# Performance work log

Measured on AMD Instinct MI355X. Metric: run time of the kernel, lower is better.

## Reference

```python
import jax, jax.numpy as jnp
import numpy as np

B, T, V, E, H = 64, 64, 32000, 512, 1024


def setup_inputs() -> dict:
    key = jax.random.key(0)
    ks = jax.random.split(key, 12)
    s = 0.02
    return {
        "hidden": jax.random.normal(ks[0], (2, B, H), jnp.float32),
        "cell": jax.random.normal(ks[1], (2, B, H), jnp.float32),
        "captions": jax.random.randint(ks[2], (B, T), 0, V, jnp.int32),
        "embed_W": jax.random.normal(ks[3], (V, E), jnp.float32) * s,
        "W_ih0": jax.random.normal(ks[4], (4 * H, E), jnp.float32) * s,
        "W_hh0": jax.random.normal(ks[5], (4 * H, H), jnp.float32) * s,
        "b_ih0": jnp.zeros((4 * H,), jnp.float32),
        "b_hh0": jnp.zeros((4 * H,), jnp.float32),
        "W_ih1": jax.random.normal(ks[6], (4 * H, H), jnp.float32) * s,
        "W_hh1": jax.random.normal(ks[7], (4 * H, H), jnp.float32) * s,
        "b_ih1": jnp.zeros((4 * H,), jnp.float32),
        "b_hh1": jnp.zeros((4 * H,), jnp.float32),
        "Wp_voc": jax.random.normal(ks[8], (V, H), jnp.float32) * s,
        "bp_voc": jnp.zeros((V,), jnp.float32),
    }


def lstm_cell(x, h, c, W_ih, W_hh, b):
    # PyTorch gate order: input, forget, cell(g), output
    gates = x @ W_ih.T + h @ W_hh.T + b  # [B, 4H]
    i, f, g, o = jnp.split(gates, 4, axis=-1)
    i, f, o = jax.nn.sigmoid(i), jax.nn.sigmoid(f), jax.nn.sigmoid(o)
    g = jnp.tanh(g)
    c_new = f * c + i * g
    h_new = o * jnp.tanh(c_new)
    return h_new, c_new


def reference(hidden, cell, captions, embed_W, W_ih0, W_hh0, b_ih0, b_hh0,
              W_ih1, W_hh1, b_ih1, b_hh1, Wp_voc, bp_voc):
    # teacher forcing (ratio=1.0): LSTM input at step t is embed(captions[:, t-1])
    x_seq = embed_W[captions[:, :-1]]        # [B, T-1, E]
    x_seq = jnp.swapaxes(x_seq, 0, 1)        # [T-1, B, E] time-major for scan
    b0 = b_ih0 + b_hh0
    b1 = b_ih1 + b_hh1

    def step(carry, x):
        h0, c0, h1, c1 = carry
        h0, c0 = lstm_cell(x, h0, c0, W_ih0, W_hh0, b0)
        h1, c1 = lstm_cell(h0, h1, c1, W_ih1, W_hh1, b1)
        logits = h1 @ Wp_voc.T + bp_voc      # [B, V]
        return (h0, c0, h1, c1), logits

    carry = (hidden[0], cell[0], hidden[1], cell[1])
    _, logits = jax.lax.scan(step, carry, x_seq)   # [T-1, B, V]
    logits = jnp.swapaxes(logits, 0, 1)            # [B, T-1, V]
    # outputs[:, 0, :] stays zero as in the torch code
    return jnp.concatenate([jnp.zeros((logits.shape[0], 1, logits.shape[2]), logits.dtype), logits], axis=1)
```

## Files before the change

### kernel.cpp

```cpp
#include <hip/hip_runtime.h>

#define B_    64
#define T_    64
#define V_    32000
#define VPAD  32768
#define E_    512
#define H_    1024
#define G4_   4096
#define TS_   63
#define MROWS 4032
#define MPAD  4096
#define BH    (B_ * H_)
#define FPAD  32

typedef __attribute__((ext_vector_type(8))) short bf16x8;
typedef __attribute__((ext_vector_type(4))) float f32x4;
typedef __attribute__((ext_vector_type(4))) unsigned int uint32x4;

__device__ __forceinline__ unsigned short bfbits(float f) {
  union { float f; unsigned int u; } cv; cv.f = f;
  unsigned int u = cv.u;
  u += 0x7fffu + ((u >> 16) & 1u);
  return (unsigned short)(u >> 16);
}
__device__ __forceinline__ float bf2f(unsigned short h) {
  union { unsigned int u; float f; } cv; cv.u = ((unsigned int)h) << 16;
  return cv.f;
}
__device__ __forceinline__ float fsig(float x) { return 1.f / (1.f + __expf(-x)); }
__device__ __forceinline__ float ftanh(float x) {
  x = fminf(fmaxf(x, -10.f), 10.f);
  const float e = __expf(2.f * x);
  return (e - 1.f) / (e + 1.f);
}

__device__ __forceinline__ void store_dword_dc(void* p, unsigned int v) {
  asm volatile("global_store_dword %0, %1, off sc0 sc1" :: "v"(p), "v"(v) : "memory");
}
__device__ __forceinline__ void store_b128_dc(void* p, uint32x4 v) {
  asm volatile("global_store_dwordx4 %0, %1, off sc0 sc1" :: "v"(p), "v"(v) : "memory");
}
__device__ __forceinline__ unsigned int load_dword_dc(const void* p) {
  unsigned int v;
  asm volatile("global_load_dword %0, %1, off sc0 sc1\n\ts_waitcnt vmcnt(0)"
               : "=v"(v) : "v"(p) : "memory");
  return v;
}
__device__ __forceinline__ void store_dword_nt(void* p, float f) {
  union { float f; unsigned int u; } cv; cv.f = f;
  asm volatile("global_store_dword %0, %1, off nt" :: "v"(p), "v"(cv.u) : "memory");
}

__device__ __forceinline__ void gload16(const void* g, void* l) {
  __builtin_amdgcn_global_load_lds(
      (const __attribute__((address_space(1))) unsigned int*)g,
      (__attribute__((address_space(3))) unsigned int*)l, 16, 0, 0);
}


__global__ void k_cast4(const float4* __restrict__ s, ushort4* __restrict__ d, int n4) {
  int i = blockIdx.x * blockDim.x + threadIdx.x;
  const int st = gridDim.x * blockDim.x;
  for (; i < n4; i += st) {
    const float4 f = s[i];
    ushort4 v;
    v.x = bfbits(f.x); v.y = bfbits(f.y); v.z = bfbits(f.z); v.w = bfbits(f.w);
    d[i] = v;
  }
}

__global__ void k_bias(const float* __restrict__ a, const float* __restrict__ b,
                       float* __restrict__ o, int n) {
  const int i = blockIdx.x * blockDim.x + threadIdx.x;
  if (i < n) o[i] = a[i] + b[i];
}

__global__ void k_gather(const float* __restrict__ embed, const int* __restrict__ caps,
                         unsigned short* __restrict__ X) {
  const int i = blockIdx.x * 256 + threadIdx.x;
  const int m = i >> 7, e4 = i & 127;
  ushort4 v;
  if (m < MROWS) {
    const int t = m >> 6, b = m & 63;
    const int idx = caps[b * T_ + t];
    const float4 f = ((const float4*)embed)[(long)idx * (E_ / 4) + e4];
    v.x = bfbits(f.x); v.y = bfbits(f.y); v.z = bfbits(f.z); v.w = bfbits(f.w);
  } else {
    v = make_ushort4(0, 0, 0, 0);
  }
  ((ushort4*)X)[i] = v;
}

__global__ void k_init(const float* __restrict__ hidden, const float* __restrict__ cell,
                       unsigned short* __restrict__ H0, unsigned short* __restrict__ H1,
                       float* __restrict__ c0, float* __restrict__ c1,
                       unsigned int* __restrict__ flags) {
  const int i = blockIdx.x * 256 + threadIdx.x;
  H0[i] = bfbits(hidden[i]);
  H1[i] = bfbits(hidden[B_ * H_ + i]);
  c0[i] = cell[i];
  c1[i] = cell[B_ * H_ + i];
  if (i < 192 * FPAD) flags[i] = 0u;
}

__global__ void k_zeropad(unsigned short* __restrict__ a, unsigned short* __restrict__ b) {
  const int i = blockIdx.x * 256 + threadIdx.x;
  a[i] = 0;
  b[i] = 0;
}

__global__ void k_zero_t0(float4* __restrict__ out4) {
  const int i = blockIdx.x * 256 + threadIdx.x;
  const int b = i / (V_ / 4), v = i - b * (V_ / 4);
  out4[(long)b * (T_ * V_ / 4) + v] = make_float4(0.f, 0.f, 0.f, 0.f);
}

template <int KDIM, bool TO_OUT, bool SWZ>
__global__ __launch_bounds__(256) void k_gemm(
    const unsigned short* __restrict__ A, const unsigned short* __restrict__ Bm,
    const float* __restrict__ bias, unsigned short* __restrict__ Cb,
    float* __restrict__ Cout, int N) {
  __shared__ unsigned short As[128 * 32];
  __shared__ unsigned short Bs[128 * 32];
  const int tid = threadIdx.x;
  const int w = tid >> 6, l = tid & 63;
  const int wm = (w >> 1) * 64, wn = (w & 1) * 64;
  const int lr = l & 15, lk = (l >> 4) * 8;
  int bx, by;
  if constexpr (SWZ) {
    const int flat = blockIdx.x;
    const int k = flat & 7, i = flat >> 3;
    bx = (k << 5) + (i >> 5);
    by = i & 31;
  } else {
    bx = blockIdx.x; by = blockIdx.y;
  }
  const long am0 = (long)by * 128;
  const long bn0 = (long)bx * 128;

  const int u0 = tid, u1 = tid + 256;
  const char* gA0 = (const char*)(A + (am0 + (u0 >> 2)) * KDIM) + (u0 & 3) * 16;
  const char* gA1 = (const char*)(A + (am0 + (u1 >> 2)) * KDIM) + (u1 & 3) * 16;
  const char* gB0 = (const char*)(Bm + (bn0 + (u0 >> 2)) * KDIM) + (u0 & 3) * 16;
  const char* gB1 = (const char*)(Bm + (bn0 + (u1 >> 2)) * KDIM) + (u1 & 3) * 16;
  char* lA0 = (char*)As + u0 * 16; char* lA1 = (char*)As + u1 * 16;
  char* lB0 = (char*)Bs + u0 * 16; char* lB1 = (char*)Bs + u1 * 16;

  f32x4 acc[4][4];
  const f32x4 z = {0.f, 0.f, 0.f, 0.f};
  #pragma unroll
  for (int mi = 0; mi < 4; ++mi)
    #pragma unroll
    for (int ni = 0; ni < 4; ++ni) acc[mi][ni] = z;

  for (int k0 = 0; k0 < KDIM; k0 += 32) {
    __syncthreads();
    gload16(gA0 + (long)k0 * 2, lA0);
    gload16(gA1 + (long)k0 * 2, lA1);
    gload16(gB0 + (long)k0 * 2, lB0);
    gload16(gB1 + (long)k0 * 2, lB1);
    __syncthreads();
    bf16x8 af[4], bfr[4];
    #pragma unroll
    for (int mi = 0; mi < 4; ++mi)
      af[mi] = *(const bf16x8*)(As + (wm + mi * 16 + lr) * 32 + lk);
    #pragma unroll
    for (int ni = 0; ni < 4; ++ni)
      bfr[ni] = *(const bf16x8*)(Bs + (wn + ni * 16 + lr) * 32 + lk);
    #pragma unroll
    for (int mi = 0; mi < 4; ++mi)
      #pragma unroll
      for (int ni = 0; ni < 4; ++ni)
        acc[mi][ni] = __builtin_amdgcn_mfma_f32_16x16x32_bf16(af[mi], bfr[ni], acc[mi][ni], 0, 0, 0);
  }

  #pragma unroll
  for (int ni = 0; ni < 4; ++ni) {
    const int n = (int)bn0 + wn + ni * 16 + lr;
    const float bv = (!TO_OUT || n < V_) ? bias[n] : 0.f;
    #pragma unroll
    for (int mi = 0; mi < 4; ++mi) {
      #pragma unroll
      for (int r = 0; r < 4; ++r) {
        const int m = (int)am0 + wm + mi * 16 + (l >> 4) * 4 + r;
        const float v = acc[mi][ni][r] + bv;
        if constexpr (TO_OUT) {
          if (m < MROWS && n < V_) {
            const int t = m >> 6, b = m & 63;
            store_dword_nt(Cout + (long)(b * T_ + t + 1) * V_ + n, v);
          }
        } else {
          Cb[(long)m * N + n] = bfbits(v);
        }
      }
    }
  }
}

__global__ __launch_bounds__(256) void k_fused(
    const unsigned short* __restrict__ Whh0b,
    const unsigned short* __restrict__ Whh1b,
    const unsigned short* __restrict__ Wih1b,
    const unsigned short* __restrict__ Xp,
    unsigned short* __restrict__ H0b,
    unsigned short* __restrict__ H1b,
    const float* __restrict__ c0i, const float* __restrict__ c1i,
    const float* __restrict__ b1s,
    unsigned int* __restrict__ f0,
    unsigned int* __restrict__ f1) {
  __shared__ unsigned short Wl[64 * 1024];
  __shared__ __align__(16) float gs1[4][64][8];
  unsigned short (*hexch)[16] = (unsigned short (*)[16])gs1;

  const int tid = threadIdx.x;
  const int w = tid >> 6, l = tid & 63;
  const int lcol = l & 15, khi = l >> 4;
  const int bw = w * 16;
  const f32x4 z = {0.f, 0.f, 0.f, 0.f};

  if (blockIdx.x < 64) {
    const int blk = blockIdx.x;
    const int jb = blk << 4;
    for (int u = tid; u < 64 * 128; u += 256) {
      const int rr = u >> 7, cu = u & 127;
      const int g = rr >> 4, jj = rr & 15;
      ((bf16x8*)Wl)[rr * 128 + (cu ^ (rr & 7))] =
          *(const bf16x8*)(Whh0b + (size_t)(g * 1024 + jb + jj) * H_ + cu * 8);
    }
    f32x4 cr;
    #pragma unroll
    for (int r = 0; r < 4; ++r)
      cr[r] = c0i[(size_t)(bw + khi * 4 + r) * H_ + jb + lcol];
    unsigned short pin[16];
    #pragma unroll
    for (int r = 0; r < 4; ++r) {
      const unsigned short* ir = Xp + (size_t)(bw + khi * 4 + r) * G4_ + jb + lcol;
      pin[r * 4 + 0] = ir[0];
      pin[r * 4 + 1] = ir[H_];
      pin[r * 4 + 2] = ir[2 * H_];
      pin[r * 4 + 3] = ir[3 * H_];
    }
    __syncthreads();

    for (int s = 0; s < TS_; ++s) {
      if (s > 0) {
        if (tid < 64)
          while (load_dword_dc(&f0[tid << 5]) < (unsigned)s)
            __builtin_amdgcn_s_sleep(1);
        __syncthreads();
      }
      f32x4 a0, a1, a2, a3;
      #pragma unroll
      for (int r = 0; r < 4; ++r) {
        a0[r] = bf2f(pin[r * 4 + 0]);
        a1[r] = bf2f(pin[r * 4 + 1]);
        a2[r] = bf2f(pin[r * 4 + 2]);
        a3[r] = bf2f(pin[r * 4 + 3]);
      }
      const unsigned short* hrow = H0b + (size_t)s * BH + (size_t)(bw + lcol) * H_ + khi * 8;
      #pragma unroll 8
      for (int kk = 0; kk < 32; ++kk) {
        const bf16x8 av = *(const bf16x8*)(hrow + kk * 32);
        const int un = (kk * 4 + khi) ^ (lcol & 7);
        const bf16x8 b0 = ((const bf16x8*)Wl)[(0 * 16 + lcol) * 128 + un];
        const bf16x8 b1 = ((const bf16x8*)Wl)[(1 * 16 + lcol) * 128 + un];
        const bf16x8 b2 = ((const bf16x8*)Wl)[(2 * 16 + lcol) * 128 + un];
        const bf16x8 b3 = ((const bf16x8*)Wl)[(3 * 16 + lcol) * 128 + un];
        a0 = __builtin_amdgcn_mfma_f32_16x16x32_bf16(av, b0, a0, 0, 0, 0);
        a1 = __builtin_amdgcn_mfma_f32_16x16x32_bf16(av, b1, a1, 0, 0, 0);
        a2 = __builtin_amdgcn_mfma_f32_16x16x32_bf16(av, b2, a2, 0, 0, 0);
        a3 = __builtin_amdgcn_mfma_f32_16x16x32_bf16(av, b3, a3, 0, 0, 0);
      }
      #pragma unroll
      for (int r = 0; r < 4; ++r) {
        const float gi = fsig(a0[r]);
        const float gf = fsig(a1[r]);
        const float gg = ftanh(a2[r]);
        const float go = fsig(a3[r]);
        cr[r] = gf * cr[r] + gi * gg;
        hexch[bw + khi * 4 + r][lcol] = bfbits(go * ftanh(cr[r]));
      }
      if (s + 1 < TS_) {
        const unsigned short* inb = Xp + (size_t)(s + 1) * (B_ * G4_);
        #pragma unroll
        for (int r = 0; r < 4; ++r) {
          const unsigned short* ir = inb + (size_t)(bw + khi * 4 + r) * G4_ + jb + lcol;
          pin[r * 4 + 0] = ir[0];
          pin[r * 4 + 1] = ir[H_];
          pin[r * 4 + 2] = ir[2 * H_];
          pin[r * 4 + 3] = ir[3 * H_];
        }
      }
      __syncthreads();
      if (tid < 128) {
        const int b = tid >> 1, hf = tid & 1;
        const uint32x4 v = *(const uint32x4*)&hexch[b][hf * 8];
        store_b128_dc(H0b + (size_t)(s + 1) * BH + (size_t)b * H_ + jb + hf * 8, v);
      }
      __syncthreads();
      if (tid == 0) store_dword_dc(&f0[blk << 5], (unsigned)(s + 1));
    }
  } else {
    const int blk1 = blockIdx.x - 64;
    const int jb1 = blk1 << 3;
    for (int u = tid; u < 64 * 128; u += 256) {
      const int pr = u >> 7, cu = u & 127;
      const int prl = pr & 31, tt = prl >> 4, lr_ = prl & 15;
      const int g = tt * 2 + (lr_ >> 3), jj = lr_ & 7;
      const unsigned short* src =
          ((pr >> 5) ? Wih1b : Whh1b) + (size_t)(g * 1024 + jb1 + jj) * H_ + cu * 8;
      ((bf16x8*)Wl)[pr * 128 + (cu ^ (pr & 7))] = *(const bf16x8*)src;
    }
    const int bb = tid >> 2;
    const int j0 = (tid * 2) & 7;
    float cA = c1i[(size_t)bb * H_ + jb1 + j0];
    float cB = c1i[(size_t)bb * H_ + jb1 + j0 + 1];
    float biA[4], biB[4];
    #pragma unroll
    for (int g = 0; g < 4; ++g) {
      biA[g] = b1s[g * 1024 + jb1 + j0];
      biB[g] = b1s[g * 1024 + jb1 + j0 + 1];
    }
    __syncthreads();

    for (int s = 1; s <= TS_; ++s) {
      {
        const unsigned t0 = (unsigned)s, t1 = (unsigned)(s - 1);
        if (tid < 64) {
          while (load_dword_dc(&f0[tid << 5]) < t0) __builtin_amdgcn_s_sleep(1);
        } else if (tid < 192) {
          while (load_dword_dc(&f1[(tid - 64) << 5]) < t1) __builtin_amdgcn_s_sleep(1);
        }
        __syncthreads();
      }
      f32x4 ac0 = z, ac1 = z;
      const unsigned short* a1p = H1b + (size_t)(s - 1) * BH + (size_t)(bw + lcol) * H_ + khi * 8;
      const unsigned short* a0p = H0b + (size_t)s * BH + (size_t)(bw + lcol) * H_ + khi * 8;
      #pragma unroll 8
      for (int kk = 0; kk < 32; ++kk) {
        const bf16x8 av = *(const bf16x8*)(a1p + kk * 32);
        const int un = (kk * 4 + khi) ^ (lcol & 7);
        const bf16x8 b0 = ((const bf16x8*)Wl)[(0 + lcol) * 128 + un];
        const bf16x8 b1 = ((const bf16x8*)Wl)[(16 + lcol) * 128 + un];
        ac0 = __builtin_amdgcn_mfma_f32_16x16x32_bf16(av, b0, ac0, 0, 0, 0);
        ac1 = __builtin_amdgcn_mfma_f32_16x16x32_bf16(av, b1, ac1, 0, 0, 0);
      }
      #pragma unroll 8
      for (int kk = 0; kk < 32; ++kk) {
        const bf16x8 av = *(const bf16x8*)(a0p + kk * 32);
        const int un = (kk * 4 + khi) ^ (lcol & 7);
        const bf16x8 b0 = ((const bf16x8*)Wl)[(32 + lcol) * 128 + un];
        const bf16x8 b1 = ((const bf16x8*)Wl)[(48 + lcol) * 128 + un];
        ac0 = __builtin_amdgcn_mfma_f32_16x16x32_bf16(av, b0, ac0, 0, 0, 0);
        ac1 = __builtin_amdgcn_mfma_f32_16x16x32_bf16(av, b1, ac1, 0, 0, 0);
      }
      #pragma unroll
      for (int r = 0; r < 4; ++r) {
        const int b = bw + khi * 4 + r;
        gs1[lcol >> 3][b][lcol & 7] = ac0[r];
        gs1[2 + (lcol >> 3)][b][lcol & 7] = ac1[r];
      }
      __syncthreads();
      {
        const float giA = fsig(gs1[0][bb][j0] + biA[0]);
        const float gfA = fsig(gs1[1][bb][j0] + biA[1]);
        const float ggA = ftanh(gs1[2][bb][j0] + biA[2]);
        const float goA = fsig(gs1[3][bb][j0] + biA[3]);
        cA = gfA * cA + giA * ggA;
        const unsigned short hA = bfbits(goA * ftanh(cA));
        const float giB = fsig(gs1[0][bb][j0 + 1] + biB[0]);
        const float gfB = fsig(gs1[1][bb][j0 + 1] + biB[1]);
        const float ggB = ftanh(gs1[2][bb][j0 + 1] + biB[2]);
        const float goB = fsig(gs1[3][bb][j0 + 1] + biB[3]);
        cB = gfB * cB + giB * ggB;
        const unsigned short hB = bfbits(goB * ftanh(cB));
        const unsigned int hv = ((unsigned int)hB << 16) | hA;
        store_dword_dc(H1b + (size_t)s * BH + (size_t)bb * H_ + jb1 + j0, hv);
      }
      __syncthreads();
      if (tid == 0) store_dword_dc(&f1[blk1 << 5], (unsigned)s);
    }
  }
}


extern "C" void kernel_launch(void* const* d_in, const int* in_sizes, int n_in,
                              void* d_out, int out_size, void* d_ws, size_t ws_size,
                              hipStream_t stream) {
  (void)in_sizes; (void)n_in; (void)out_size; (void)ws_size;
  const float* hidden = (const float*)d_in[0];
  const float* cell   = (const float*)d_in[1];
  const int*   caps   = (const int*)d_in[2];
  const float* embed  = (const float*)d_in[3];
  const float* Wih0   = (const float*)d_in[4];
  const float* Whh0   = (const float*)d_in[5];
  const float* bih0   = (const float*)d_in[6];
  const float* bhh0   = (const float*)d_in[7];
  const float* Wih1   = (const float*)d_in[8];
  const float* Whh1   = (const float*)d_in[9];
  const float* bih1   = (const float*)d_in[10];
  const float* bhh1   = (const float*)d_in[11];
  const float* Wp     = (const float*)d_in[12];
  const float* bp     = (const float*)d_in[13];
  float* out = (float*)d_out;

  char* p = (char*)d_ws;
  auto alloc = [&](size_t bytes) { char* r = p; p += (bytes + 255) & ~(size_t)255; return r; };
  unsigned short* Xbf   = (unsigned short*)alloc((size_t)MPAD * E_ * 2);
  unsigned short* Wih0b = (unsigned short*)alloc((size_t)G4_ * E_ * 2);
  unsigned short* Whh0b = (unsigned short*)alloc((size_t)G4_ * H_ * 2);
  unsigned short* Wih1b = (unsigned short*)alloc((size_t)G4_ * H_ * 2);
  unsigned short* Whh1b = (unsigned short*)alloc((size_t)G4_ * H_ * 2);
  unsigned short* Wpb   = (unsigned short*)alloc((size_t)VPAD * H_ * 2);
  unsigned short* Xp    = (unsigned short*)alloc((size_t)MPAD * G4_ * 2);
  unsigned short* H0    = (unsigned short*)alloc((size_t)(MPAD + B_) * H_ * 2);
  unsigned short* H1    = (unsigned short*)alloc((size_t)(MPAD + B_) * H_ * 2);
  float* c0  = (float*)alloc((size_t)B_ * H_ * 4);
  float* c1  = (float*)alloc((size_t)B_ * H_ * 4);
  float* b0s = (float*)alloc((size_t)G4_ * 4);
  float* b1s = (float*)alloc((size_t)G4_ * 4);
  unsigned int* cbar = (unsigned int*)alloc((size_t)192 * FPAD * 4);

  k_cast4<<<2048, 256, 0, stream>>>((const float4*)Wih0, (ushort4*)Wih0b, G4_ * E_ / 4);
  k_cast4<<<2048, 256, 0, stream>>>((const float4*)Whh0, (ushort4*)Whh0b, G4_ * H_ / 4);
  k_cast4<<<2048, 256, 0, stream>>>((const float4*)Wih1, (ushort4*)Wih1b, G4_ * H_ / 4);
  k_cast4<<<2048, 256, 0, stream>>>((const float4*)Whh1, (ushort4*)Whh1b, G4_ * H_ / 4);
  k_cast4<<<4096, 256, 0, stream>>>((const float4*)Wp,   (ushort4*)Wpb,   V_ * H_ / 4);
  k_bias<<<16, 256, 0, stream>>>(bih0, bhh0, b0s, G4_);
  k_bias<<<16, 256, 0, stream>>>(bih1, bhh1, b1s, G4_);
  k_gather<<<2048, 256, 0, stream>>>(embed, caps, Xbf);
  k_init<<<256, 256, 0, stream>>>(hidden, cell, H0, H1, c0, c1, cbar);
  k_zeropad<<<256, 256, 0, stream>>>(H0 + (size_t)MPAD * H_, H1 + (size_t)MPAD * H_);
  k_zero_t0<<<2000, 256, 0, stream>>>((float4*)out);

  k_gemm<512, false, false><<<dim3(32, 32), 256, 0, stream>>>(Xbf, Wih0b, b0s, Xp, nullptr, G4_);

  k_fused<<<192, 256, 0, stream>>>(Whh0b, Whh1b, Wih1b, Xp, H0, H1, c0, c1, b1s,
                                   cbar, cbar + 64 * FPAD);

  k_gemm<1024, true, true><<<8192, 256, 0, stream>>>(H1 + (size_t)B_ * H_, Wpb, bp, nullptr, out, V_);
}
```

Baseline: 1.114 ms.

## Shrink persistent LSTM kernel to 48 blocks streaming weights from L2

```diff
diff --git a/kernel.cpp b/kernel.cpp
--- a/kernel.cpp
+++ b/kernel.cpp
@@ -49,6 +49,12 @@
 __device__ __forceinline__ void store_dword_nt(void* p, float f) {
   union { float f; unsigned int u; } cv; cv.f = f;
   asm volatile("global_store_dword %0, %1, off nt" :: "v"(p), "v"(cv.u) : "memory");
+}
+__device__ __forceinline__ bf16x8 ldnt8(const unsigned short* p) {
+  return __builtin_nontemporal_load((const bf16x8*)p);
+}
+__device__ __forceinline__ unsigned short ldnt1(const unsigned short* p) {
+  return __builtin_nontemporal_load(p);
 }
 
 __device__ __forceinline__ void gload16(const void* g, void* l) {
@@ -208,174 +214,166 @@
     const float* __restrict__ b1s,
     unsigned int* __restrict__ f0,
     unsigned int* __restrict__ f1) {
-  __shared__ unsigned short Wl[64 * 1024];
-  __shared__ __align__(16) float gs1[4][64][8];
-  unsigned short (*hexch)[16] = (unsigned short (*)[16])gs1;
-
+  __shared__ unsigned short hex0[64][64];
   const int tid = threadIdx.x;
   const int w = tid >> 6, l = tid & 63;
-  const int lcol = l & 15, khi = l >> 4;
-  const int bw = w * 16;
-  const f32x4 z = {0.f, 0.f, 0.f, 0.f};
-
-  if (blockIdx.x < 64) {
-    const int blk = blockIdx.x;
-    const int jb = blk << 4;
-    for (int u = tid; u < 64 * 128; u += 256) {
-      const int rr = u >> 7, cu = u & 127;
-      const int g = rr >> 4, jj = rr & 15;
-      ((bf16x8*)Wl)[rr * 128 + (cu ^ (rr & 7))] =
-          *(const bf16x8*)(Whh0b + (size_t)(g * 1024 + jb + jj) * H_ + cu * 8);
+  const int lr = l & 15, khi = l >> 4;
+  const int wm = w >> 1, wn = w & 1;
+  const int bw = wm * 32;
+
+  if (blockIdx.x < 16) {
+    const int blk = blockIdx.x, jb = blk << 6;
+    float cr[16];
+    #pragma unroll
+    for (int mf = 0; mf < 2; ++mf)
+      #pragma unroll
+      for (int js = 0; js < 2; ++js)
+        #pragma unroll
+        for (int r = 0; r < 4; ++r)
+          cr[(mf * 2 + js) * 4 + r] =
+              c0i[(size_t)(bw + mf * 16 + khi * 4 + r) * H_ + jb + wn * 32 + js * 16 + lr];
+    const unsigned short* wb[8];
+    #pragma unroll
+    for (int nf = 0; nf < 8; ++nf) {
+      const int g = nf >> 1, js = nf & 1;
+      wb[nf] = Whh0b + (size_t)(g * 1024 + jb + wn * 32 + js * 16 + lr) * H_ + khi * 8;
     }
-    f32x4 cr;
-    #pragma unroll
-    for (int r = 0; r < 4; ++r)
-      cr[r] = c0i[(size_t)(bw + khi * 4 + r) * H_ + jb + lcol];
-    unsigned short pin[16];
-    #pragma unroll
-    for (int r = 0; r < 4; ++r) {
-      const unsigned short* ir = Xp + (size_t)(bw + khi * 4 + r) * G4_ + jb + lcol;
-      pin[r * 4 + 0] = ir[0];
-      pin[r * 4 + 1] = ir[H_];
-      pin[r * 4 + 2] = ir[2 * H_];
-      pin[r * 4 + 3] = ir[3 * H_];
-    }
-    __syncthreads();
 
     for (int s = 0; s < TS_; ++s) {
       if (s > 0) {
-        if (tid < 64)
-          while (load_dword_dc(&f0[tid << 5]) < (unsigned)s)
-            __builtin_amdgcn_s_sleep(1);
+        if (tid < 16)
+          while (load_dword_dc(&f0[tid << 5]) < (unsigned)s) __builtin_amdgcn_s_sleep(1);
         __syncthreads();
       }
-      f32x4 a0, a1, a2, a3;
-      #pragma unroll
-      for (int r = 0; r < 4; ++r) {
-        a0[r] = bf2f(pin[r * 4 + 0]);
-        a1[r] = bf2f(pin[r * 4 + 1]);
-        a2[r] = bf2f(pin[r * 4 + 2]);
-        a3[r] = bf2f(pin[r * 4 + 3]);
-      }
-      const unsigned short* hrow = H0b + (size_t)s * BH + (size_t)(bw + lcol) * H_ + khi * 8;
-      #pragma unroll 8
+      const unsigned short* xs = Xp + (size_t)s * (B_ * G4_);
+      f32x4 acc[2][8];
+      #pragma unroll
+      for (int mf = 0; mf < 2; ++mf)
+        #pragma unroll
+        for (int nf = 0; nf < 8; ++nf) {
+          const int g = nf >> 1, js = nf & 1;
+          const size_t cb = (size_t)(g * 1024 + jb + wn * 32 + js * 16 + lr);
+          #pragma unroll
+          for (int r = 0; r < 4; ++r)
+            acc[mf][nf][r] = bf2f(ldnt1(xs + (size_t)(bw + mf * 16 + khi * 4 + r) * G4_ + cb));
+        }
+      const unsigned short* a0p = H0b + (size_t)s * BH + (size_t)(bw + lr) * H_ + khi * 8;
+      const unsigned short* a1p = a0p + 16 * H_;
+      #pragma unroll 4
       for (int kk = 0; kk < 32; ++kk) {
-        const bf16x8 av = *(const bf16x8*)(hrow + kk * 32);
-        const int un = (kk * 4 + khi) ^ (lcol & 7);
-        const bf16x8 b0 = ((const bf16x8*)Wl)[(0 * 16 + lcol) * 128 + un];
-        const bf16x8 b1 = ((const bf16x8*)Wl)[(1 * 16 + lcol) * 128 + un];
-        const bf16x8 b2 = ((const bf16x8*)Wl)[(2 * 16 + lcol) * 128 + un];
-        const bf16x8 b3 = ((const bf16x8*)Wl)[(3 * 16 + lcol) * 128 + un];
-        a0 = __builtin_amdgcn_mfma_f32_16x16x32_bf16(av, b0, a0, 0, 0, 0);
-        a1 = __builtin_amdgcn_mfma_f32_16x16x32_bf16(av, b1, a1, 0, 0, 0);
-        a2 = __builtin_amdgcn_mfma_f32_16x16x32_bf16(av, b2, a2, 0, 0, 0);
-        a3 = __builtin_amdgcn_mfma_f32_16x16x32_bf16(av, b3, a3, 0, 0, 0);
-      }
-      #pragma unroll
-      for (int r = 0; r < 4; ++r) {
-        const float gi = fsig(a0[r]);
-        const float gf = fsig(a1[r]);
-        const float gg = ftanh(a2[r]);
-        const float go = fsig(a3[r]);
-        cr[r] = gf * cr[r] + gi * gg;
-        hexch[bw + khi * 4 + r][lcol] = bfbits(go * ftanh(cr[r]));
-      }
-      if (s + 1 < TS_) {
-        const unsigned short* inb = Xp + (size_t)(s + 1) * (B_ * G4_);
-        #pragma unroll
-        for (int r = 0; r < 4; ++r) {
-          const unsigned short* ir = inb + (size_t)(bw + khi * 4 + r) * G4_ + jb + lcol;
-          pin[r * 4 + 0] = ir[0];
-          pin[r * 4 + 1] = ir[H_];
-          pin[r * 4 + 2] = ir[2 * H_];
-          pin[r * 4 + 3] = ir[3 * H_];
-        }
-      }
+        const bf16x8 av0 = ldnt8(a0p + kk * 32);
+        const bf16x8 av1 = ldnt8(a1p + kk * 32);
+        #pragma unroll
+        for (int nf = 0; nf < 8; ++nf) {
+          const bf16x8 bv = *(const bf16x8*)(wb[nf] + kk * 32);
+          acc[0][nf] = __builtin_amdgcn_mfma_f32_16x16x32_bf16(av0, bv, acc[0][nf], 0, 0, 0);
+          acc[1][nf] = __builtin_amdgcn_mfma_f32_16x16x32_bf16(av1, bv, acc[1][nf], 0, 0, 0);
+        }
+      }
+      #pragma unroll
+      for (int mf = 0; mf < 2; ++mf)
+        #pragma unroll
+        for (int js = 0; js < 2; ++js)
+          #pragma unroll
+          for (int r = 0; r < 4; ++r) {
+            const int ci = (mf * 2 + js) * 4 + r;
+            const float gi = fsig(acc[mf][0 + js][r]);
+            const float gf = fsig(acc[mf][2 + js][r]);
+            const float gg = ftanh(acc[mf][4 + js][r]);
+            const float go = fsig(acc[mf][6 + js][r]);
+            cr[ci] = gf * cr[ci] + gi * gg;
+            hex0[bw + mf * 16 + khi * 4 + r][wn * 32 + js * 16 + lr] = bfbits(go * ftanh(cr[ci]));
+          }
       __syncthreads();
-      if (tid < 128) {
-        const int b = tid >> 1, hf = tid & 1;
-        const uint32x4 v = *(const uint32x4*)&hexch[b][hf * 8];
-        store_b128_dc(H0b + (size_t)(s + 1) * BH + (size_t)b * H_ + jb + hf * 8, v);
+      {
+        unsigned short* hop = H0b + (size_t)(s + 1) * BH;
+        const int v0 = tid, v1 = tid + 256;
+        store_b128_dc(hop + (size_t)(v0 >> 3) * H_ + jb + (v0 & 7) * 8,
+                      *(const uint32x4*)&hex0[v0 >> 3][(v0 & 7) * 8]);
+        store_b128_dc(hop + (size_t)(v1 >> 3) * H_ + jb + (v1 & 7) * 8,
+                      *(const uint32x4*)&hex0[v1 >> 3][(v1 & 7) * 8]);
       }
       __syncthreads();
       if (tid == 0) store_dword_dc(&f0[blk << 5], (unsigned)(s + 1));
     }
   } else {
-    const int blk1 = blockIdx.x - 64;
-    const int jb1 = blk1 << 3;
-    for (int u = tid; u < 64 * 128; u += 256) {
-      const int pr = u >> 7, cu = u & 127;
-      const int prl = pr & 31, tt = prl >> 4, lr_ = prl & 15;
-      const int g = tt * 2 + (lr_ >> 3), jj = lr_ & 7;
-      const unsigned short* src =
-          ((pr >> 5) ? Wih1b : Whh1b) + (size_t)(g * 1024 + jb1 + jj) * H_ + cu * 8;
-      ((bf16x8*)Wl)[pr * 128 + (cu ^ (pr & 7))] = *(const bf16x8*)src;
+    const int blk1 = blockIdx.x - 16, jb1 = blk1 << 5;
+    float cr[8];
+    #pragma unroll
+    for (int mf = 0; mf < 2; ++mf)
+      #pragma unroll
+      for (int r = 0; r < 4; ++r)
+        cr[mf * 4 + r] = c1i[(size_t)(bw + mf * 16 + khi * 4 + r) * H_ + jb1 + wn * 16 + lr];
+    const unsigned short* wbh[4];
+    const unsigned short* wbx[4];
+    float bi[4];
+    #pragma unroll
+    for (int g = 0; g < 4; ++g) {
+      const size_t wr = (size_t)(g * 1024 + jb1 + wn * 16 + lr);
+      wbh[g] = Whh1b + wr * H_ + khi * 8;
+      wbx[g] = Wih1b + wr * H_ + khi * 8;
+      bi[g] = b1s[g * 1024 + jb1 + wn * 16 + lr];
     }
-    const int bb = tid >> 2;
-    const int j0 = (tid * 2) & 7;
-    float cA = c1i[(size_t)bb * H_ + jb1 + j0];
-    float cB = c1i[(size_t)bb * H_ + jb1 + j0 + 1];
-    float biA[4], biB[4];
-    #pragma unroll
-    for (int g = 0; g < 4; ++g) {
-      biA[g] = b1s[g * 1024 + jb1 + j0];
-      biB[g] = b1s[g * 1024 + jb1 + j0 + 1];
-    }
-    __syncthreads();
 
     for (int s = 1; s <= TS_; ++s) {
-      {
-        const unsigned t0 = (unsigned)s, t1 = (unsigned)(s - 1);
-        if (tid < 64) {
-          while (load_dword_dc(&f0[tid << 5]) < t0) __builtin_amdgcn_s_sleep(1);
-        } else if (tid < 192) {
-          while (load_dword_dc(&f1[(tid - 64) << 5]) < t1) __builtin_amdgcn_s_sleep(1);
-        }
-        __syncthreads();
-      }
-      f32x4 ac0 = z, ac1 = z;
-      const unsigned short* a1p = H1b + (size_t)(s - 1) * BH + (size_t)(bw + lcol) * H_ + khi * 8;
-      const unsigned short* a0p = H0b + (size_t)s * BH + (size_t)(bw + lcol) * H_ + khi * 8;
-      #pragma unroll 8
+      if (tid < 32) {
+        while (load_dword_dc(&f1[tid << 5]) < (unsigned)(s - 1)) __builtin_amdgcn_s_sleep(1);
+      } else if (tid < 48) {
+        while (load_dword_dc(&f0[(tid - 32) << 5]) < (unsigned)s) __builtin_amdgcn_s_sleep(1);
+      }
+      __syncthreads();
+      f32x4 acc[2][4];
+      #pragma unroll
+      for (int mf = 0; mf < 2; ++mf)
+        #pragma unroll
+        for (int g = 0; g < 4; ++g) {
+          f32x4 v; v[0] = bi[g]; v[1] = bi[g]; v[2] = bi[g]; v[3] = bi[g];
+          acc[mf][g] = v;
+        }
+      const unsigned short* h1p0 = H1b + (size_t)(s - 1) * BH + (size_t)(bw + lr) * H_ + khi * 8;
+      const unsigned short* h1p1 = h1p0 + 16 * H_;
+      #pragma unroll 4
       for (int kk = 0; kk < 32; ++kk) {
-        const bf16x8 av = *(const bf16x8*)(a1p + kk * 32);
-        const int un = (kk * 4 + khi) ^ (lcol & 7);
-        const bf16x8 b0 = ((const bf16x8*)Wl)[(0 + lcol) * 128 + un];
-        const bf16x8 b1 = ((const bf16x8*)Wl)[(16 + lcol) * 128 + un];
-        ac0 = __builtin_amdgcn_mfma_f32_16x16x32_bf16(av, b0, ac0, 0, 0, 0);
-        ac1 = __builtin_amdgcn_mfma_f32_16x16x32_bf16(av, b1, ac1, 0, 0, 0);
-      }
-      #pragma unroll 8
+        const bf16x8 av0 = ldnt8(h1p0 + kk * 32);
+        const bf16x8 av1 = ldnt8(h1p1 + kk * 32);
+        #pragma unroll
+        for (int g = 0; g < 4; ++g) {
+          const bf16x8 bv = *(const bf16x8*)(wbh[g] + kk * 32);
+          acc[0][g] = __builtin_amdgcn_mfma_f32_16x16x32_bf16(av0, bv, acc[0][g], 0, 0, 0);
+          acc[1][g] = __builtin_amdgcn_mfma_f32_16x16x32_bf16(av1, bv, acc[1][g], 0, 0, 0);
+        }
+      }
+      const unsigned short* h0p0 = H0b + (size_t)s * BH + (size_t)(bw + lr) * H_ + khi * 8;
+      const unsigned short* h0p1 = h0p0 + 16 * H_;
+      #pragma unroll 4
       for (int kk = 0; kk < 32; ++kk) {
-        const bf16x8 av = *(const bf16x8*)(a0p + kk * 32);
-        const int un = (kk * 4 + khi) ^ (lcol & 7);
-        const bf16x8 b0 = ((const bf16x8*)Wl)[(32 + lcol) * 128 + un];
-        const bf16x8 b1 = ((const bf16x8*)Wl)[(48 + lcol) * 128 + un];
-        ac0 = __builtin_amdgcn_mfma_f32_16x16x32_bf16(av, b0, ac0, 0, 0, 0);
-        ac1 = __builtin_amdgcn_mfma_f32_16x16x32_bf16(av, b1, ac1, 0, 0, 0);
-      }
-      #pragma unroll
-      for (int r = 0; r < 4; ++r) {
-        const int b = bw + khi * 4 + r;
-        gs1[lcol >> 3][b][lcol & 7] = ac0[r];
-        gs1[2 + (lcol >> 3)][b][lcol & 7] = ac1[r];
-      }
+        const bf16x8 av0 = ldnt8(h0p0 + kk * 32);
+        const bf16x8 av1 = ldnt8(h0p1 + kk * 32);
+        #pragma unroll
+        for (int g = 0; g < 4; ++g) {
+          const bf16x8 bv = *(const bf16x8*)(wbx[g] + kk * 32);
+          acc[0][g] = __builtin_amdgcn_mfma_f32_16x16x32_bf16(av0, bv, acc[0][g], 0, 0, 0);
+          acc[1][g] = __builtin_amdgcn_mfma_f32_16x16x32_bf16(av1, bv, acc[1][g], 0, 0, 0);
+        }
+      }
+      #pragma unroll
+      for (int mf = 0; mf < 2; ++mf)
+        #pragma unroll
+        for (int r = 0; r < 4; ++r) {
+          const int ci = mf * 4 + r;
+          const float gi = fsig(acc[mf][0][r]);
+          const float gf = fsig(acc[mf][1][r]);
+          const float gg = ftanh(acc[mf][2][r]);
+          const float go = fsig(acc[mf][3][r]);
+          cr[ci] = gf * cr[ci] + gi * gg;
+          hex0[bw + mf * 16 + khi * 4 + r][wn * 16 + lr] = bfbits(go * ftanh(cr[ci]));
+        }
       __syncthreads();
       {
-        const float giA = fsig(gs1[0][bb][j0] + biA[0]);
-        const float gfA = fsig(gs1[1][bb][j0] + biA[1]);
-        const float ggA = ftanh(gs1[2][bb][j0] + biA[2]);
-        const float goA = fsig(gs1[3][bb][j0] + biA[3]);
-        cA = gfA * cA + giA * ggA;
-        const unsigned short hA = bfbits(goA * ftanh(cA));
-        const float giB = fsig(gs1[0][bb][j0 + 1] + biB[0]);
-        const float gfB = fsig(gs1[1][bb][j0 + 1] + biB[1]);
-        const float ggB = ftanh(gs1[2][bb][j0 + 1] + biB[2]);
-        const float goB = fsig(gs1[3][bb][j0 + 1] + biB[3]);
-        cB = gfB * cB + giB * ggB;
-        const unsigned short hB = bfbits(goB * ftanh(cB));
-        const unsigned int hv = ((unsigned int)hB << 16) | hA;
-        store_dword_dc(H1b + (size_t)s * BH + (size_t)bb * H_ + jb1 + j0, hv);
+        unsigned short* hop = H1b + (size_t)s * BH;
+        const int u = tid;
+        store_b128_dc(hop + (size_t)(u >> 2) * H_ + jb1 + (u & 3) * 8,
+                      *(const uint32x4*)&hex0[u >> 2][(u & 3) * 8]);
       }
       __syncthreads();
       if (tid == 0) store_dword_dc(&f1[blk1 << 5], (unsigned)s);
@@ -435,8 +433,8 @@
 
   k_gemm<512, false, false><<<dim3(32, 32), 256, 0, stream>>>(Xbf, Wih0b, b0s, Xp, nullptr, G4_);
 
-  k_fused<<<192, 256, 0, stream>>>(Whh0b, Whh1b, Wih1b, Xp, H0, H1, c0, c1, b1s,
-                                   cbar, cbar + 64 * FPAD);
+  k_fused<<<48, 256, 0, stream>>>(Whh0b, Whh1b, Wih1b, Xp, H0, H1, c0, c1, b1s,
+                                  cbar, cbar + 64 * FPAD);
 
   k_gemm<1024, true, true><<<8192, 256, 0, stream>>>(H1 + (size_t)B_ * H_, Wpb, bp, nullptr, out, V_);
 }
```

Result: slower. 3.974 ms (+256.7%).
